# Kernel optimization log

Measured on AMD Instinct MI355X. Metric: run time of the kernel, lower is better.

Reference implementation:

```python
import jax, jax.numpy as jnp
import numpy as np

IN_FEATURES = 512
OUT_FEATURES = 256
BATCH = 1024


def setup_inputs() -> dict:
    key = jax.random.key(0)
    k1, k2, k3, k4 = jax.random.split(key, 4)
    n_lower = IN_FEATURES * (IN_FEATURES - 1) // 2  # strictly-lower triangle count
    return {
        "inputs": jax.random.normal(k1, (BATCH, IN_FEATURES), dtype=jnp.float32),
        "weight": jax.random.normal(k2, (OUT_FEATURES, 1, IN_FEATURES), dtype=jnp.float32),
        "L_diags": jax.random.uniform(k3, (OUT_FEATURES, IN_FEATURES), dtype=jnp.float32),
        "L_lower": jax.random.normal(k4, (OUT_FEATURES, n_lower), dtype=jnp.float32) * 0.05,
    }


def _build_L(L_diags, L_lower):
    # Per-class lower-triangular matrix: diag = L_diags**2, strict lower = L_lower.
    K, d = L_diags.shape
    ri, ci = np.tril_indices(d, k=-1)  # static index pattern (row-major, matches torch.tril_indices)
    diag_idx = jnp.arange(d)
    L = jnp.zeros((K, d, d), dtype=L_diags.dtype)
    L = L.at[:, diag_idx, diag_idx].set(jnp.square(L_diags))
    L = L.at[:, ri, ci].set(L_lower)
    return L  # [K, d, d]


def reference(inputs, weight, L_diags, L_lower):
    L = _build_L(L_diags, L_lower)                      # [K, d, d]
    pinputs = jnp.einsum('bd,kde->kbe', inputs, L)      # [K, B, d]
    pweights = jnp.einsum('kod,kde->koe', weight, L)    # [K, 1, d]
    dist = pinputs - pweights                           # broadcast over B -> [K, B, d]
    out = jnp.sqrt(jnp.sum(jnp.square(dist), axis=2))   # torch.norm(dim=2) -> [K, B]
    return out.T                                        # [B, K]
```

## Files before the change

### kernel.cpp

```cpp
#include <hip/hip_runtime.h>
#include <hip/hip_bf16.h>
#include <math.h>

#define B_SZ   1024
#define D_SZ   512
#define KC_SZ  256
#define NLOW   130816

#define STEP_ELEMS  8192
#define NSTEPS      20
#define CLASS_ELEMS (NSTEPS * STEP_ELEMS)

#define OFF_XP     (size_t)(KC_SZ * CLASS_ELEMS * 2)
#define OFF_TPART  (OFF_XP + 64 * STEP_ELEMS * 2)
#define OFF_T      (OFF_TPART + (size_t)KC_SZ * 8 * 512 * 4)
#define WS_NEED    (OFF_T + (size_t)KC_SZ * 512 * 4)

typedef __attribute__((ext_vector_type(4))) float  f32x4;
typedef __attribute__((ext_vector_type(8))) __bf16 bf16x8;

__global__ __launch_bounds__(256)
void prep_x(const float* __restrict__ X, __hip_bfloat16* __restrict__ Xp) {
    const int pg  = blockIdx.x;
    const int mt  = pg >> 3, kch = pg & 7;
    __bf16* out = (__bf16*)Xp + (size_t)pg * STEP_ELEMS;
    const int tid = threadIdx.x;
    #pragma unroll
    for (int i = 0; i < 4; ++i) {
        const int line = tid + i * 256;
        const int wmg = line >> 9, mi = (line >> 7) & 3, h = (line >> 6) & 1;
        const int lane = line & 63, q = lane >> 4, c = lane & 15;
        const int row = mt * 128 + wmg * 64 + mi * 16 + c;
        const float* src = X + (size_t)row * D_SZ + kch * 64 + h * 32 + q * 8;
        f32x4 v0 = ((const f32x4*)src)[0];
        f32x4 v1 = ((const f32x4*)src)[1];
        bf16x8 p;
        #pragma unroll
        for (int j = 0; j < 4; ++j) { p[j] = (__bf16)v0[j]; p[j + 4] = (__bf16)v1[j]; }
        *(bf16x8*)(out + line * 8) = p;
    }
}

__device__ __forceinline__ int sbase_of(int ct) { return ct * (9 - ct); }

__global__ __launch_bounds__(256)
void prep_b(const float* __restrict__ Ldiag,
            const float* __restrict__ Llow,
            const float* __restrict__ W,
            __hip_bfloat16* __restrict__ Bp,
            float* __restrict__ tpart) {
    __shared__ float Ls[64][65];
    __shared__ float Wsm[64];
    __shared__ float pt[4][64];

    const int bid = blockIdx.x;
    const int kc  = bid >> 6;
    const int et  = (bid >> 3) & 7;
    const int dt  = bid & 7;
    const int ct  = et >> 1;
    const int dmin = ct << 1;
    if (dt < dmin) return;

    const int s  = sbase_of(ct) + (dt - dmin);
    const int e0 = et << 6, d0 = dt << 6;
    const int tid = threadIdx.x;

    __bf16* page = (__bf16*)Bp + (size_t)kc * CLASS_ELEMS + (size_t)s * STEP_ELEMS;
    float*  tp   = tpart + ((size_t)(kc * 8 + dt)) * 512;

    const int qp = tid >> 5;
    const int ep = tid & 31;
    const int el0 = ((et & 1) << 6) + (ep << 1);
    const int h = qp >> 2, q = qp & 3;
    const int line0 = ((((el0 >> 6) * 4 + ((el0 >> 4) & 3)) * 2 + h) * 64) + q * 16 + (el0 & 15);
    __bf16* dst = page + line0 * 8;

    if (d0 + 64 <= e0) {
        bf16x8 z;
        #pragma unroll
        for (int i = 0; i < 8; ++i) z[i] = (__bf16)0.f;
        *(bf16x8*)dst = z;
        *(bf16x8*)(dst + 8) = z;
        if (tid < 64) tp[et * 64 + tid] = 0.f;
        return;
    }

    if (tid < 64) Wsm[tid] = W[(size_t)kc * D_SZ + d0 + tid];

    const int r  = tid >> 2;
    const int cq = (tid & 3) << 4;
    const float* lowb = Llow + (size_t)kc * NLOW;
    const int d   = d0 + r;
    const int tri = (d * (d - 1)) >> 1;

    if (d0 >= e0 + 64) {
        #pragma unroll
        for (int j = 0; j < 16; ++j) Ls[r][cq + j] = lowb[tri + e0 + cq + j];
    } else {
        const float* diagb = Ldiag + (size_t)kc * D_SZ;
        #pragma unroll
        for (int j = 0; j < 16; ++j) {
            const int e = e0 + cq + j;
            float v = 0.f;
            if (e < d)       v = lowb[tri + e];
            else if (e == d) { float qd = diagb[d]; v = qd * qd; }
            Ls[r][cq + j] = v;
        }
    }
    __syncthreads();

    bf16x8 p0, p1;
    #pragma unroll
    for (int j = 0; j < 8; ++j) {
        p0[j] = (__bf16)Ls[qp * 8 + j][ep * 2];
        p1[j] = (__bf16)Ls[qp * 8 + j][ep * 2 + 1];
    }
    *(bf16x8*)dst = p0;
    *(bf16x8*)(dst + 8) = p1;

    {
        const int part = tid >> 6, ei = tid & 63;
        float sum = 0.f;
        #pragma unroll
        for (int j = 0; j < 16; ++j)
            sum += Wsm[part * 16 + j] * Ls[part * 16 + j][ei];
        pt[part][ei] = sum;
    }
    __syncthreads();
    if (tid < 64)
        tp[et * 64 + tid] = pt[0][tid] + pt[1][tid] + pt[2][tid] + pt[3][tid];
}

__global__ __launch_bounds__(256)
void t_reduce(const float* __restrict__ tpart, float* __restrict__ Tv) {
    const int idx = blockIdx.x * 256 + threadIdx.x;
    const int kc = idx >> 9, e = idx & 511;
    const int ct = e >> 7;
    float s = 0.f;
    for (int dt = ct << 1; dt < 8; ++dt)
        s += tpart[((size_t)(kc * 8 + dt)) * 512 + e];
    Tv[idx] = s;
}

__device__ __forceinline__ int kch_of(int s) {
    return (s < 8) ? s : (s < 14) ? s - 6 : (s < 18) ? s - 10 : s - 12;
}

__global__ __launch_bounds__(256, 2)
void gml2_main(const __hip_bfloat16* __restrict__ Xp,
               const __hip_bfloat16* __restrict__ Bp,
               const float* __restrict__ Tv,
               float* __restrict__ Out) {
    __shared__ float osum[2][128];

    const int tid = threadIdx.x;
    const int bx  = blockIdx.x;
    const int xcd = bx & 7;
    const int g   = bx >> 3;
    const int kc  = xcd * 32 + (g >> 3);
    const int mt  = g & 7;

    const int lane = tid & 63;
    const int wave = tid >> 6;
    const int wmg  = wave & 1;
    const int wng  = wave >> 1;
    const int c    = lane & 15;
    const int q    = lane >> 4;

    const __bf16* pA = (const __bf16*)Xp + (size_t)(mt * 8) * STEP_ELEMS;
    const __bf16* pB = (const __bf16*)Bp + (size_t)kc * CLASS_ELEMS;

    int aoff[4][2], boff[4][2];
    #pragma unroll
    for (int mi = 0; mi < 4; ++mi)
        #pragma unroll
        for (int h = 0; h < 2; ++h)
            aoff[mi][h] = ((((wmg * 4 + mi) * 2 + h) * 64) + lane) * 8;
    #pragma unroll
    for (int ni = 0; ni < 4; ++ni)
        #pragma unroll
        for (int h = 0; h < 2; ++h)
            boff[ni][h] = ((((wng * 4 + ni) * 2 + h) * 64) + lane) * 8;

    f32x4 acc[4][4];
    #pragma unroll
    for (int mi = 0; mi < 4; ++mi)
        #pragma unroll
        for (int ni = 0; ni < 4; ++ni)
            acc[mi][ni] = (f32x4){0.f, 0.f, 0.f, 0.f};
    float rsum[16];
    #pragma unroll
    for (int i = 0; i < 16; ++i) rsum[i] = 0.f;

    bf16x8 fa0[4][2], fb0[4][2], fa1[4][2], fb1[4][2];

#define LOAD_A(FA, KCH) { const __bf16* p_ = pA + (KCH) * STEP_ELEMS;          \
    _Pragma("unroll") for (int mi = 0; mi < 4; ++mi)                           \
    _Pragma("unroll") for (int h = 0; h < 2; ++h)                              \
        FA[mi][h] = *(const bf16x8*)(p_ + aoff[mi][h]); }
#define LOAD_B(FB, SP) { const __bf16* p_ = pB + (SP) * STEP_ELEMS;            \
    _Pragma("unroll") for (int ni = 0; ni < 4; ++ni)                           \
    _Pragma("unroll") for (int h = 0; h < 2; ++h)                              \
        FB[ni][h] = *(const bf16x8*)(p_ + boff[ni][h]); }
#define MFMA_STEP(FA, FB)                                                      \
    _Pragma("unroll") for (int mi = 0; mi < 4; ++mi)                           \
    _Pragma("unroll") for (int ni = 0; ni < 4; ++ni)                           \
    _Pragma("unroll") for (int h = 0; h < 2; ++h)                              \
        acc[mi][ni] = __builtin_amdgcn_mfma_f32_16x16x32_bf16(                 \
            FA[mi][h], FB[ni][h], acc[mi][ni], 0, 0, 0);

#define FOLD(CT) {                                                             \
    float tv_[4];                                                              \
    _Pragma("unroll") for (int ni = 0; ni < 4; ++ni)                           \
        tv_[ni] = Tv[kc * 512 + (CT) * 128 + wng * 64 + ni * 16 + c];          \
    _Pragma("unroll") for (int mi = 0; mi < 4; ++mi)                           \
    _Pragma("unroll") for (int ni = 0; ni < 4; ++ni)                           \
    _Pragma("unroll") for (int r = 0; r < 4; ++r) {                            \
        float y_ = acc[mi][ni][r] - tv_[ni];                                   \
        rsum[mi * 4 + r] += y_ * y_;                                           \
        acc[mi][ni][r] = 0.f; } }

    LOAD_A(fa0, 0); LOAD_B(fb0, 0);

    for (int s = 0; s < NSTEPS; s += 2) {
        if (s == 8)       { FOLD(0); }
        else if (s == 14) { FOLD(1); }
        else if (s == 18) { FOLD(2); }

        LOAD_A(fa1, kch_of(s + 1)); LOAD_B(fb1, s + 1);
        MFMA_STEP(fa0, fb0);
        if (s + 2 < NSTEPS) { LOAD_A(fa0, kch_of(s + 2)); LOAD_B(fb0, s + 2); }
        MFMA_STEP(fa1, fb1);
    }
    FOLD(3);

    #pragma unroll
    for (int i = 0; i < 16; ++i) {
        float v = rsum[i];
        v += __shfl_xor(v, 1, 64);
        v += __shfl_xor(v, 2, 64);
        v += __shfl_xor(v, 4, 64);
        v += __shfl_xor(v, 8, 64);
        rsum[i] = v;
    }
    if (c == 0) {
        #pragma unroll
        for (int mi = 0; mi < 4; ++mi)
            #pragma unroll
            for (int r = 0; r < 4; ++r)
                osum[wng][wmg * 64 + mi * 16 + q * 4 + r] = rsum[mi * 4 + r];
    }
    __syncthreads();
    if (tid < 128) {
        float v = osum[0][tid] + osum[1][tid];
        Out[(size_t)(mt * 128 + tid) * KC_SZ + kc] = sqrtf(v);
    }
}

#define FLDA 40
#define BM 128
#define BN 128
__device__ __forceinline__ void fstep_map(int s, int& ct, int& k0) {
    if (s < 16)      { ct = 0; k0 = s * 32; }
    else if (s < 28) { ct = 1; k0 = 128 + (s - 16) * 32; }
    else if (s < 36) { ct = 2; k0 = 256 + (s - 28) * 32; }
    else             { ct = 3; k0 = 384 + (s - 36) * 32; }
}
__global__ __launch_bounds__(256, 2)
void gml2_fallback(const float* __restrict__ X, const float* __restrict__ W,
                   const float* __restrict__ Ldiag, const float* __restrict__ Llow,
                   float* __restrict__ Out) {
    __shared__ __bf16 As[BM * FLDA];
    __shared__ __bf16 Bs[BN * FLDA];
    __shared__ float  Ws[D_SZ];
    __shared__ float  osum[2][BM];
    const int tid = threadIdx.x;
    const int bx  = blockIdx.x;
    const int xcd = bx & 7;
    const int g   = bx >> 3;
    const int kc  = xcd * 32 + (g >> 3);
    const int mt  = g & 7;
    const int lane = tid & 63, wave = tid >> 6;
    const int wm = (wave & 1) * 64, wn = (wave >> 1) * 64;
    const int c = lane & 15, q = lane >> 4;
    const int am = tid >> 1, akh = (tid & 1) << 4;
    const float* xrow = X + (size_t)(mt * BM + am) * D_SZ;
    const float* wrow = W + (size_t)kc * D_SZ;
    const int be = tid & 127, bd = (tid >> 7) << 4;
    const float* lowbase  = Llow  + (size_t)kc * NLOW;
    const float* diagbase = Ldiag + (size_t)kc * D_SZ;
    if (tid < 128) ((f32x4*)Ws)[tid] = ((const f32x4*)wrow)[tid];
    float rsum[16];
    #pragma unroll
    for (int i = 0; i < 16; ++i) rsum[i] = 0.f;
    f32x4 acc[4][4];
    #pragma unroll
    for (int mi = 0; mi < 4; ++mi)
        #pragma unroll
        for (int ni = 0; ni < 4; ++ni) acc[mi][ni] = (f32x4){0.f, 0.f, 0.f, 0.f};
    f32x4 xr[4];
    float bb[16];
    auto prefetch = [&](int s) {
        int pct, pk0; fstep_map(s, pct, pk0);
        const int pe0 = pct * BN;
        const float* xp = xrow + pk0 + akh;
        #pragma unroll
        for (int i = 0; i < 4; ++i) xr[i] = ((const f32x4*)xp)[i];
        const int e = pe0 + be, d0 = pk0 + bd;
        int tri = (d0 * (d0 - 1)) >> 1;
        if (pk0 >= pe0 + BN) {
            #pragma unroll
            for (int j = 0; j < 16; ++j) { bb[j] = lowbase[tri + e]; tri += d0 + j; }
        } else {
            #pragma unroll
            for (int j = 0; j < 16; ++j) {
                const int d = d0 + j;
                float val = 0.f;
                if (d > e)       val = lowbase[tri + e];
                else if (d == e) { float dq = diagbase[d]; val = dq * dq; }
                bb[j] = val; tri += d;
            }
        }
    };
    prefetch(0);
    __syncthreads();
    int cur_ct = 0;
    for (int s = 0; s < 40; ++s) {
        int ct, k0; fstep_map(s, ct, k0);
        if (ct != cur_ct) {
            #pragma unroll
            for (int mi = 0; mi < 4; ++mi)
                #pragma unroll
                for (int ni = 0; ni < 4; ++ni)
                    #pragma unroll
                    for (int r = 0; r < 4; ++r) {
                        float y = acc[mi][ni][r];
                        rsum[mi * 4 + r] += y * y;
                        acc[mi][ni][r] = 0.f;
                    }
            cur_ct = ct;
        }
        bf16x8 ap0, ap1;
        {
            const f32x4* wsp = (const f32x4*)&Ws[k0 + akh];
            #pragma unroll
            for (int i = 0; i < 4; ++i) {
                f32x4 wv = wsp[i];
                #pragma unroll
                for (int l = 0; l < 4; ++l) {
                    float v = xr[i][l] - wv[l];
                    int idx = i * 4 + l;
                    if (idx < 8) ap0[idx] = (__bf16)v;
                    else         ap1[idx - 8] = (__bf16)v;
                }
            }
        }
        bf16x8 bp0, bp1;
        #pragma unroll
        for (int j = 0; j < 8; ++j) { bp0[j] = (__bf16)bb[j]; bp1[j] = (__bf16)bb[j + 8]; }
        __syncthreads();
        *(bf16x8*)&As[am * FLDA + akh]     = ap0;
        *(bf16x8*)&As[am * FLDA + akh + 8] = ap1;
        *(bf16x8*)&Bs[be * FLDA + bd]      = bp0;
        *(bf16x8*)&Bs[be * FLDA + bd + 8]  = bp1;
        if (s + 1 < 40) prefetch(s + 1);
        __syncthreads();
        bf16x8 af[4], bfr[4];
        #pragma unroll
        for (int mi = 0; mi < 4; ++mi)
            af[mi] = *(const bf16x8*)&As[(wm + mi * 16 + c) * FLDA + q * 8];
        #pragma unroll
        for (int ni = 0; ni < 4; ++ni)
            bfr[ni] = *(const bf16x8*)&Bs[(wn + ni * 16 + c) * FLDA + q * 8];
        #pragma unroll
        for (int mi = 0; mi < 4; ++mi)
            #pragma unroll
            for (int ni = 0; ni < 4; ++ni)
                acc[mi][ni] = __builtin_amdgcn_mfma_f32_16x16x32_bf16(
                    af[mi], bfr[ni], acc[mi][ni], 0, 0, 0);
    }
    #pragma unroll
    for (int mi = 0; mi < 4; ++mi)
        #pragma unroll
        for (int ni = 0; ni < 4; ++ni)
            #pragma unroll
            for (int r = 0; r < 4; ++r) {
                float y = acc[mi][ni][r];
                rsum[mi * 4 + r] += y * y;
            }
    #pragma unroll
    for (int i = 0; i < 16; ++i) {
        float s = rsum[i];
        s += __shfl_xor(s, 1, 64);
        s += __shfl_xor(s, 2, 64);
        s += __shfl_xor(s, 4, 64);
        s += __shfl_xor(s, 8, 64);
        rsum[i] = s;
    }
    const int wnIdx = wave >> 1;
    if (c == 0) {
        #pragma unroll
        for (int mi = 0; mi < 4; ++mi)
            #pragma unroll
            for (int r = 0; r < 4; ++r)
                osum[wnIdx][wm + mi * 16 + q * 4 + r] = rsum[mi * 4 + r];
    }
    __syncthreads();
    if (tid < BM) {
        float s = osum[0][tid] + osum[1][tid];
        Out[(size_t)(mt * BM + tid) * KC_SZ + kc] = sqrtf(s);
    }
}

extern "C" void kernel_launch(void* const* d_in, const int* in_sizes, int n_in,
                              void* d_out, int out_size, void* d_ws, size_t ws_size,
                              hipStream_t stream) {
    const float* X  = (const float*)d_in[0];
    const float* W  = (const float*)d_in[1];
    const float* Ld = (const float*)d_in[2];
    const float* Ll = (const float*)d_in[3];
    float* Out = (float*)d_out;

    if (ws_size >= WS_NEED) {
        __hip_bfloat16* Bp    = (__hip_bfloat16*)d_ws;
        __hip_bfloat16* Xp    = (__hip_bfloat16*)((char*)d_ws + OFF_XP);
        float*          tpart = (float*)((char*)d_ws + OFF_TPART);
        float*          Tvv   = (float*)((char*)d_ws + OFF_T);
        prep_x  <<<dim3(64),            dim3(256), 0, stream>>>(X, Xp);
        prep_b  <<<dim3(KC_SZ * 64),    dim3(256), 0, stream>>>(Ld, Ll, W, Bp, tpart);
        t_reduce<<<dim3(512),           dim3(256), 0, stream>>>(tpart, Tvv);
        gml2_main<<<dim3(KC_SZ * 8),    dim3(256), 0, stream>>>(Xp, Bp, Tvv, Out);
    } else {
        gml2_fallback<<<dim3(KC_SZ * 8), dim3(256), 0, stream>>>(X, W, Ld, Ll, Out);
    }
}
```

Baseline: 358.7 us.

## Restructure weight packing to one block per K-step page with vectorized loads

prep_b now launches one block per (step, class) page covering a 128x64 tile instead of 64x64 tiles, with early-exit blocks removed. Each thread loads two adjacent rows with unaligned float4 reads, packs bf16 pairs into a swizzled LDS tile, and writes the page with coalesced 16-byte stores. The W·L partial sums are reduced in LDS per 128-column slice. prep_x is split across 4x more blocks to raise parallelism. The aim is to cut launch waste and improve the memory efficiency of the preprocessing, which dominates total time over the main GEMM.

```diff
diff --git a/kernel.cpp b/kernel.cpp
--- a/kernel.cpp
+++ b/kernel.cpp
@@ -17,31 +17,32 @@
 #define WS_NEED    (OFF_T + (size_t)KC_SZ * 512 * 4)
 
 typedef __attribute__((ext_vector_type(4))) float  f32x4;
+typedef __attribute__((ext_vector_type(4), aligned(4))) float f32x4u;
 typedef __attribute__((ext_vector_type(8))) __bf16 bf16x8;
+
+__device__ __forceinline__ int sbase_of(int ct) { return ct * (9 - ct); }
+__device__ __forceinline__ int kch_of(int s) {
+    return (s < 8) ? s : (s < 14) ? s - 6 : (s < 18) ? s - 10 : s - 12;
+}
 
 __global__ __launch_bounds__(256)
 void prep_x(const float* __restrict__ X, __hip_bfloat16* __restrict__ Xp) {
-    const int pg  = blockIdx.x;
+    const int bx  = blockIdx.x;
+    const int pg  = bx >> 2;
     const int mt  = pg >> 3, kch = pg & 7;
     __bf16* out = (__bf16*)Xp + (size_t)pg * STEP_ELEMS;
-    const int tid = threadIdx.x;
-    #pragma unroll
-    for (int i = 0; i < 4; ++i) {
-        const int line = tid + i * 256;
-        const int wmg = line >> 9, mi = (line >> 7) & 3, h = (line >> 6) & 1;
-        const int lane = line & 63, q = lane >> 4, c = lane & 15;
-        const int row = mt * 128 + wmg * 64 + mi * 16 + c;
-        const float* src = X + (size_t)row * D_SZ + kch * 64 + h * 32 + q * 8;
-        f32x4 v0 = ((const f32x4*)src)[0];
-        f32x4 v1 = ((const f32x4*)src)[1];
-        bf16x8 p;
-        #pragma unroll
-        for (int j = 0; j < 4; ++j) { p[j] = (__bf16)v0[j]; p[j + 4] = (__bf16)v1[j]; }
-        *(bf16x8*)(out + line * 8) = p;
-    }
-}
-
-__device__ __forceinline__ int sbase_of(int ct) { return ct * (9 - ct); }
+    const int line = threadIdx.x + (bx & 3) * 256;
+    const int wmg = line >> 9, mi = (line >> 7) & 3, h = (line >> 6) & 1;
+    const int lane = line & 63, q = lane >> 4, c = lane & 15;
+    const int row = mt * 128 + wmg * 64 + mi * 16 + c;
+    const float* src = X + (size_t)row * D_SZ + kch * 64 + h * 32 + q * 8;
+    f32x4 v0 = ((const f32x4*)src)[0];
+    f32x4 v1 = ((const f32x4*)src)[1];
+    bf16x8 p;
+    #pragma unroll
+    for (int j = 0; j < 4; ++j) { p[j] = (__bf16)v0[j]; p[j + 4] = (__bf16)v1[j]; }
+    *(bf16x8*)(out + line * 8) = p;
+}
 
 __global__ __launch_bounds__(256)
 void prep_b(const float* __restrict__ Ldiag,
@@ -49,86 +50,90 @@
             const float* __restrict__ W,
             __hip_bfloat16* __restrict__ Bp,
             float* __restrict__ tpart) {
-    __shared__ float Ls[64][65];
-    __shared__ float Wsm[64];
-    __shared__ float pt[4][64];
-
-    const int bid = blockIdx.x;
-    const int kc  = bid >> 6;
-    const int et  = (bid >> 3) & 7;
-    const int dt  = bid & 7;
-    const int ct  = et >> 1;
-    const int dmin = ct << 1;
-    if (dt < dmin) return;
-
-    const int s  = sbase_of(ct) + (dt - dmin);
-    const int e0 = et << 6, d0 = dt << 6;
+    __shared__ __bf16 Lt[128 * 64];
+    __shared__ float  ptl[32 * 129];
+
+    const int s  = blockIdx.x;
+    const int kc = blockIdx.y;
+    const int ct = (s < 8) ? 0 : (s < 14) ? 1 : (s < 18) ? 2 : 3;
+    const int dt = kch_of(s);
+    const int e0 = ct << 7, d0 = dt << 6;
+
     const int tid = threadIdx.x;
+    const int m   = tid & 31;
+    const int seg = tid >> 5;
+    const int es  = seg << 4;
+    const int dg0 = d0 + 2 * m;
+
+    int cls;
+    if (dt >= 2 * ct + 2)      cls = 0;
+    else if (dt == 2 * ct + 1) cls = (seg < 4) ? 0 : 1;
+    else                       cls = (seg < 4) ? 1 : 2;
+
+    const float* lowb = Llow + (size_t)kc * NLOW;
+    const float2 wv = *(const float2*)(W + (size_t)kc * D_SZ + dg0);
+
+    float v0[16], v1[16];
+    if (cls == 0) {
+        const int t0 = (dg0 * (dg0 - 1)) >> 1;
+        const int t1 = t0 + dg0;
+        const float* s0 = lowb + t0 + e0 + es;
+        const float* s1 = lowb + t1 + e0 + es;
+        #pragma unroll
+        for (int i = 0; i < 4; ++i) {
+            f32x4u a = ((const f32x4u*)s0)[i];
+            f32x4u b = ((const f32x4u*)s1)[i];
+            #pragma unroll
+            for (int j = 0; j < 4; ++j) { v0[i * 4 + j] = a[j]; v1[i * 4 + j] = b[j]; }
+        }
+    } else if (cls == 1) {
+        const int t0 = (dg0 * (dg0 - 1)) >> 1;
+        const int t1 = t0 + dg0;
+        const float* diagb = Ldiag + (size_t)kc * D_SZ;
+        float q0 = diagb[dg0],     q1 = diagb[dg0 + 1];
+        q0 *= q0; q1 *= q1;
+        #pragma unroll
+        for (int j = 0; j < 16; ++j) {
+            const int eg = e0 + es + j;
+            v0[j] = (eg < dg0)     ? lowb[t0 + eg] : ((eg == dg0)     ? q0 : 0.f);
+            v1[j] = (eg < dg0 + 1) ? lowb[t1 + eg] : ((eg == dg0 + 1) ? q1 : 0.f);
+        }
+    } else {
+        #pragma unroll
+        for (int j = 0; j < 16; ++j) { v0[j] = 0.f; v1[j] = 0.f; }
+    }
+
+    char* ltb = (char*)Lt;
+    #pragma unroll
+    for (int j = 0; j < 16; ++j) {
+        const int el = es + j;
+        union { __bf16 h[2]; unsigned u; } pk;
+        pk.h[0] = (__bf16)v0[j];
+        pk.h[1] = (__bf16)v1[j];
+        const int off = el * 128 + ((4 * m) ^ ((el & 7) << 4));
+        *(unsigned*)(ltb + off) = pk.u;
+        ptl[m * 129 + el] = wv.x * v0[j] + wv.y * v1[j];
+    }
+    __syncthreads();
 
     __bf16* page = (__bf16*)Bp + (size_t)kc * CLASS_ELEMS + (size_t)s * STEP_ELEMS;
-    float*  tp   = tpart + ((size_t)(kc * 8 + dt)) * 512;
-
-    const int qp = tid >> 5;
-    const int ep = tid & 31;
-    const int el0 = ((et & 1) << 6) + (ep << 1);
-    const int h = qp >> 2, q = qp & 3;
-    const int line0 = ((((el0 >> 6) * 4 + ((el0 >> 4) & 3)) * 2 + h) * 64) + q * 16 + (el0 & 15);
-    __bf16* dst = page + line0 * 8;
-
-    if (d0 + 64 <= e0) {
-        bf16x8 z;
-        #pragma unroll
-        for (int i = 0; i < 8; ++i) z[i] = (__bf16)0.f;
-        *(bf16x8*)dst = z;
-        *(bf16x8*)(dst + 8) = z;
-        if (tid < 64) tp[et * 64 + tid] = 0.f;
-        return;
-    }
-
-    if (tid < 64) Wsm[tid] = W[(size_t)kc * D_SZ + d0 + tid];
-
-    const int r  = tid >> 2;
-    const int cq = (tid & 3) << 4;
-    const float* lowb = Llow + (size_t)kc * NLOW;
-    const int d   = d0 + r;
-    const int tri = (d * (d - 1)) >> 1;
-
-    if (d0 >= e0 + 64) {
-        #pragma unroll
-        for (int j = 0; j < 16; ++j) Ls[r][cq + j] = lowb[tri + e0 + cq + j];
-    } else {
-        const float* diagb = Ldiag + (size_t)kc * D_SZ;
-        #pragma unroll
-        for (int j = 0; j < 16; ++j) {
-            const int e = e0 + cq + j;
-            float v = 0.f;
-            if (e < d)       v = lowb[tri + e];
-            else if (e == d) { float qd = diagb[d]; v = qd * qd; }
-            Ls[r][cq + j] = v;
-        }
-    }
-    __syncthreads();
-
-    bf16x8 p0, p1;
-    #pragma unroll
-    for (int j = 0; j < 8; ++j) {
-        p0[j] = (__bf16)Ls[qp * 8 + j][ep * 2];
-        p1[j] = (__bf16)Ls[qp * 8 + j][ep * 2 + 1];
-    }
-    *(bf16x8*)dst = p0;
-    *(bf16x8*)(dst + 8) = p1;
-
-    {
-        const int part = tid >> 6, ei = tid & 63;
+    const int lane = tid & 63, q = lane >> 4, c = lane & 15;
+    #pragma unroll
+    for (int k = 0; k < 4; ++k) {
+        const int ln = k * 256 + tid;
+        const int up = ln >> 6;
+        const int h  = up & 1;
+        const int el = ((up >> 3) << 6) + (((up >> 1) & 3) << 4) + c;
+        const int off = el * 128 + (((h << 6) + (q << 4)) ^ ((el & 7) << 4));
+        *(bf16x8*)(page + (size_t)ln * 8) = *(const bf16x8*)(ltb + off);
+    }
+
+    if (tid < 128) {
         float sum = 0.f;
         #pragma unroll
-        for (int j = 0; j < 16; ++j)
-            sum += Wsm[part * 16 + j] * Ls[part * 16 + j][ei];
-        pt[part][ei] = sum;
-    }
-    __syncthreads();
-    if (tid < 64)
-        tp[et * 64 + tid] = pt[0][tid] + pt[1][tid] + pt[2][tid] + pt[3][tid];
+        for (int mm = 0; mm < 32; ++mm) sum += ptl[mm * 129 + tid];
+        tpart[((size_t)(kc * 8 + dt)) * 512 + e0 + tid] = sum;
+    }
 }
 
 __global__ __launch_bounds__(256)
@@ -140,10 +145,6 @@
     for (int dt = ct << 1; dt < 8; ++dt)
         s += tpart[((size_t)(kc * 8 + dt)) * 512 + e];
     Tv[idx] = s;
-}
-
-__device__ __forceinline__ int kch_of(int s) {
-    return (s < 8) ? s : (s < 14) ? s - 6 : (s < 18) ? s - 10 : s - 12;
 }
 
 __global__ __launch_bounds__(256, 2)
@@ -426,8 +427,8 @@
         __hip_bfloat16* Xp    = (__hip_bfloat16*)((char*)d_ws + OFF_XP);
         float*          tpart = (float*)((char*)d_ws + OFF_TPART);
         float*          Tvv   = (float*)((char*)d_ws + OFF_T);
-        prep_x  <<<dim3(64),            dim3(256), 0, stream>>>(X, Xp);
-        prep_b  <<<dim3(KC_SZ * 64),    dim3(256), 0, stream>>>(Ld, Ll, W, Bp, tpart);
+        prep_x  <<<dim3(256),           dim3(256), 0, stream>>>(X, Xp);
+        prep_b  <<<dim3(NSTEPS, KC_SZ), dim3(256), 0, stream>>>(Ld, Ll, W, Bp, tpart);
         t_reduce<<<dim3(512),           dim3(256), 0, stream>>>(tpart, Tvv);
         gml2_main<<<dim3(KC_SZ * 8),    dim3(256), 0, stream>>>(Xp, Bp, Tvv, Out);
     } else {
```

Result: faster. 327.4 us (-8.7%).
